# Kernel tuning notes

Hardware: AMD Instinct MI355X
Metric: run time of the kernel (lower is better)

The kernel has to match this reference:

```python
import jax, jax.numpy as jnp
import numpy as np

WH, WW = 16, 16          # window_size
C = 384                  # in_channel
H = 12                   # num_heads
HD = C // H              # head_dim = 32
B = 256                  # num_windows * batch
N = WH * WW              # tokens per window = 256
CPB_HID = 512


def _build_buffers():
    # relative_coords_table: [1, 2*WH-1, 2*WW-1, 2], log-spaced coords (pretrain_window_size = [0,0])
    rch = np.arange(-(WH - 1), WH, dtype=np.float32)
    rcw = np.arange(-(WW - 1), WW, dtype=np.float32)
    table = np.stack(np.meshgrid(rch, rcw, indexing='ij'), axis=-1)[None]  # [1,2WH-1,2WW-1,2]
    table[..., 0] /= (WH - 1)
    table[..., 1] /= (WW - 1)
    table = np.sign(table) * np.log2(np.abs(table) + 1.0) / np.log2(8)
    # relative_position_index: [N, N] int indices into flattened table
    ch = np.arange(WH)
    cw = np.arange(WW)
    coords = np.stack(np.meshgrid(ch, cw, indexing='ij'))      # [2, WH, WW]
    cf = coords.reshape(2, -1)                                  # [2, N]
    rel = cf[:, :, None] - cf[:, None, :]                       # [2, N, N]
    rel = rel.transpose(1, 2, 0).astype(np.int64)               # [N, N, 2]
    rel[..., 0] += WH - 1
    rel[..., 1] += WW - 1
    rel[..., 0] *= 2 * WW - 1
    rpi = rel.sum(-1)                                           # [N, N]
    return jnp.asarray(table, jnp.float32), jnp.asarray(rpi, jnp.int32)


def setup_inputs() -> dict:
    key = jax.random.key(0)
    ks = jax.random.split(key, 9)
    table, rpi = _build_buffers()
    return {
        'x': jax.random.normal(ks[0], (B, N, C), jnp.float32),
        'qkv_w': jax.random.normal(ks[1], (3 * C, C), jnp.float32) * 0.02,
        'q_bias': jnp.zeros((C,), jnp.float32),
        'v_bias': jnp.zeros((C,), jnp.float32),
        'logit_scale': jnp.log(10.0 * jnp.ones((H, 1, 1), jnp.float32)),
        'cpb_w1': jax.random.normal(ks[2], (CPB_HID, 2), jnp.float32) * 0.02,
        'cpb_b1': jnp.zeros((CPB_HID,), jnp.float32),
        'cpb_w2': jax.random.normal(ks[3], (H, CPB_HID), jnp.float32) * 0.02,
        'proj_w': jax.random.normal(ks[4], (C, C), jnp.float32) * 0.02,
        'proj_b': jnp.zeros((C,), jnp.float32),
        'rel_coords_table': table,
        'rel_pos_index': rpi,
    }


def reference(x, qkv_w, q_bias, v_bias, logit_scale, cpb_w1, cpb_b1, cpb_w2,
              proj_w, proj_b, rel_coords_table, rel_pos_index):
    b, n, c = x.shape
    h, hd = H, c // H
    # qkv with q/v bias, zero k bias
    bias = jnp.concatenate([q_bias, jnp.zeros_like(v_bias), v_bias])
    qkv = x @ qkv_w.T + bias                                   # [B,N,3C]
    qkv = qkv.reshape(b, n, 3, h, hd).transpose(2, 0, 3, 1, 4)  # [3,B,H,N,hd]
    q, k, v = qkv[0], qkv[1], qkv[2]
    # cosine attention: L2-normalize q, k (F.normalize with eps=1e-12)
    qn = q / jnp.maximum(jnp.linalg.norm(q, axis=-1, keepdims=True), 1e-12)
    kn = k / jnp.maximum(jnp.linalg.norm(k, axis=-1, keepdims=True), 1e-12)
    attn = jnp.einsum('bhnd,bhmd->bhnm', qn, kn)               # [B,H,N,N]
    # learnable per-head logit scale, clamped at log(1/0.01)
    scale = jnp.exp(jnp.minimum(logit_scale, jnp.log(100.0)))  # [H,1,1]
    attn = attn * scale
    # continuous relative position bias MLP: 2 -> 512 -> H
    hid = jax.nn.relu(rel_coords_table @ cpb_w1.T + cpb_b1)    # [1,2WH-1,2WW-1,512]
    bias_table = (hid @ cpb_w2.T).reshape(-1, h)               # [(2WH-1)*(2WW-1), H]
    rpb = bias_table[rel_pos_index.reshape(-1)].reshape(n, n, h).transpose(2, 0, 1)
    rpb = 16.0 * jax.nn.sigmoid(rpb)                           # [H,N,N]
    attn = jax.nn.softmax(attn + rpb, axis=-1)
    out = jnp.einsum('bhnm,bhmd->bhnd', attn, v)               # [B,H,N,hd]
    out = out.transpose(0, 2, 1, 3).reshape(b, n, c)
    return out @ proj_w.T + proj_b
```

## Files before the change

kernel.cpp:

```cpp
#include <hip/hip_runtime.h>

typedef unsigned int uint;
typedef unsigned short ushort_t;
typedef ushort_t ushort8 __attribute__((ext_vector_type(8)));
typedef ushort_t ushort4v __attribute__((ext_vector_type(4)));
typedef short short8 __attribute__((ext_vector_type(8)));
typedef float floatx4 __attribute__((ext_vector_type(4)));

#define WSQ 25165824L
#define NH  12
#define NT  256
#define HD  32

__device__ __forceinline__ float bf2f(ushort_t u) {
    uint x = ((uint)u) << 16;
    return __builtin_bit_cast(float, x);
}
__device__ __forceinline__ ushort_t f2bf(float f) {
    uint u = __builtin_bit_cast(uint, f);
    uint lsb = (u >> 16) & 1u;
    return (ushort_t)((u + 0x7FFFu + lsb) >> 16);
}
__device__ __forceinline__ float ld1(const void* p, long i, int f) {
    return f ? ((const float*)p)[i] : bf2f(((const ushort_t*)p)[i]);
}

__global__ void detect_kernel(const ushort_t* __restrict__ x, int* __restrict__ flag) {
    int t = threadIdx.x;
    uint u = x[2 * t];
    int e = (u >> 7) & 0xFF;
    int weird = (e > 147 || e < 107) ? 1 : 0;
    unsigned long long b = __ballot(weird);
    if (t == 0) *flag = (__popcll(b) > 19) ? 1 : 0;
}

__global__ __launch_bounds__(256) void cvt_kernel(
    const void* __restrict__ src, ushort_t* __restrict__ dst,
    const int* __restrict__ fl, long n8)
{
    long i = (long)blockIdx.x * 256 + threadIdx.x;
    if (i >= n8) return;
    if (*fl) {
        const floatx4* s = (const floatx4*)((const float*)src + i * 8);
        floatx4 a = s[0], b = s[1];
        ushort8 o;
        for (int j = 0; j < 4; ++j) { o[j] = f2bf(a[j]); o[4 + j] = f2bf(b[j]); }
        *(ushort8*)(dst + i * 8) = o;
    } else {
        *(ushort8*)(dst + i * 8) = *(const ushort8*)((const ushort_t*)src + i * 8);
    }
}

__global__ __launch_bounds__(512) void cpb_kernel(
    const void* __restrict__ tab, const void* __restrict__ w1,
    const void* __restrict__ b1, const void* __restrict__ w2,
    const int* __restrict__ fl, float* __restrict__ bt)
{
    __shared__ float hid[512];
    const int f = *fl;
    int p = blockIdx.x, j = threadIdx.x;
    float c0 = ld1(tab, p * 2 + 0, f);
    float c1 = ld1(tab, p * 2 + 1, f);
    float v = ld1(w1, j * 2 + 0, f) * c0 + ld1(w1, j * 2 + 1, f) * c1 + ld1(b1, j, f);
    hid[j] = fmaxf(v, 0.0f);
    __syncthreads();
    if (j < NH) {
        float s = 0.0f;
        for (int i = 0; i < 512; ++i) s += hid[i] * ld1(w2, (long)j * 512 + i, f);
        bt[p * NH + j] = s;
    }
}

__global__ __launch_bounds__(256) void rpb_kernel(
    const int* __restrict__ rpi, const float* __restrict__ bt,
    float* __restrict__ rpb)
{
    int idx = blockIdx.x * 256 + threadIdx.x;
    int h = idx >> 16, ij = idx & 65535;
    float x = bt[rpi[ij] * NH + h];
    rpb[idx] = 16.0f / (1.0f + __expf(-x));
}

template <int MODE>
__global__ __launch_bounds__(256) void gemm_bt(
    const ushort_t* __restrict__ A, const ushort_t* __restrict__ Bw,
    const void* __restrict__ bias0, const void* __restrict__ bias2,
    void* __restrict__ Cout, const int* __restrict__ fl)
{
    const int K = 384;
    __shared__ ushort_t As[128 * 72];
    __shared__ ushort_t Bs[128 * 72];
    const int f = *fl;
    const int tid = threadIdx.x;
    const int w = tid >> 6, lane = tid & 63, l15 = lane & 15, quad = lane >> 4;
    const int m0 = blockIdx.y * 128, n0 = blockIdx.x * 128;
    const int rw = (w >> 1) * 64, cw = (w & 1) * 64;
    const int lr = tid >> 3, lc = (tid & 7) * 8;

    floatx4 acc[4][4] = {};
    ushort8 pa[4], pb[4];

    for (int i = 0; i < 4; ++i) {
        int r = lr + i * 32;
        if (MODE == 0) {
            pa[i] = *(const ushort8*)&A[(long)(m0 + r) * K + lc];
        } else {
            int m = m0 + r, kc = lc;
            long ad = ((long)(m >> 8) * 12 + (kc >> 5)) * 8192 + (m & 255) * 32 + (kc & 31);
            pa[i] = *(const ushort8*)&A[ad];
        }
        pb[i] = *(const ushort8*)&Bw[(long)(n0 + r) * K + lc];
    }

    for (int kt = 0; kt < K; kt += 64) {
        for (int i = 0; i < 4; ++i) {
            int r = lr + i * 32;
            *(ushort8*)&As[r * 72 + lc] = pa[i];
            *(ushort8*)&Bs[r * 72 + lc] = pb[i];
        }
        __syncthreads();
        if (kt + 64 < K) {
            for (int i = 0; i < 4; ++i) {
                int r = lr + i * 32;
                if (MODE == 0) {
                    pa[i] = *(const ushort8*)&A[(long)(m0 + r) * K + kt + 64 + lc];
                } else {
                    int m = m0 + r, kc = kt + 64 + lc;
                    long ad = ((long)(m >> 8) * 12 + (kc >> 5)) * 8192 + (m & 255) * 32 + (kc & 31);
                    pa[i] = *(const ushort8*)&A[ad];
                }
                pb[i] = *(const ushort8*)&Bw[(long)(n0 + r) * K + kt + 64 + lc];
            }
        }
        for (int ks = 0; ks < 64; ks += 32) {
            short8 af[4], bfr[4];
            for (int mt = 0; mt < 4; ++mt)
                af[mt] = *(short8*)&As[(rw + mt * 16 + l15) * 72 + ks + quad * 8];
            for (int nt = 0; nt < 4; ++nt)
                bfr[nt] = *(short8*)&Bs[(cw + nt * 16 + l15) * 72 + ks + quad * 8];
            for (int mt = 0; mt < 4; ++mt)
                for (int nt = 0; nt < 4; ++nt)
                    acc[mt][nt] = __builtin_amdgcn_mfma_f32_16x16x32_bf16(
                        af[mt], bfr[nt], acc[mt][nt], 0, 0, 0);
        }
        __syncthreads();
    }

    for (int mt = 0; mt < 4; ++mt) {
        for (int nt = 0; nt < 4; ++nt) {
            int c = n0 + cw + nt * 16 + l15;
            if (MODE == 0) {
                int which = c / 384, cc = c % 384;
                float bias = (which == 0) ? ld1(bias0, cc, f)
                           : (which == 2) ? ld1(bias2, cc, f) : 0.0f;
                int hh = cc >> 5, dd = cc & 31;
                for (int r = 0; r < 4; ++r) {
                    int m = m0 + rw + mt * 16 + quad * 4 + r;
                    int b = m >> 8, ntok = m & 255;
                    long dst = (long)which * WSQ +
                               (((long)(b * NH + hh) * NT + ntok) * HD + dd);
                    ((ushort_t*)Cout)[dst] = f2bf(acc[mt][nt][r] + bias);
                }
            } else {
                float bias = ld1(bias0, c, f);
                for (int r = 0; r < 4; ++r) {
                    int m = m0 + rw + mt * 16 + quad * 4 + r;
                    float v = acc[mt][nt][r] + bias;
                    long o = (long)m * 384 + c;
                    if (f) ((float*)Cout)[o] = v;
                    else   ((ushort_t*)Cout)[o] = f2bf(v);
                }
            }
        }
    }
}

__global__ __launch_bounds__(128) void attn_kernel(
    ushort_t* __restrict__ qkv, const void* __restrict__ ls,
    const float* __restrict__ rpb, const int* __restrict__ fl)
{
    __shared__ ushort_t ks[256 * 40];
    __shared__ ushort_t vts[32 * 264];
    __shared__ ushort_t ps[2 * 16 * 264];

    const int f = *fl;
    const int bh = blockIdx.x;
    const int b = bh / NH, h = bh % NH;
    ushort_t* qp = qkv + (long)bh * NT * HD;
    const ushort_t* kp = qp + WSQ;
    const ushort_t* vp = qp + 2 * WSQ;
    const int tid = threadIdx.x;
    const float scale = __expf(fminf(ld1(ls, h, f), 4.6051702f));

    for (int t = tid; t < 256; t += 128) {
        ushort8 kv[4];
        for (int i = 0; i < 4; ++i) kv[i] = *(const ushort8*)&kp[t * HD + i * 8];
        float fv[32]; float ss = 0.0f;
        for (int i = 0; i < 4; ++i)
            for (int j = 0; j < 8; ++j) {
                float v = bf2f(kv[i][j]); fv[i * 8 + j] = v; ss += v * v;
            }
        float rn = 1.0f / fmaxf(sqrtf(ss), 1e-12f);
        for (int i = 0; i < 4; ++i) {
            ushort8 o;
            for (int j = 0; j < 8; ++j) o[j] = f2bf(fv[i * 8 + j] * rn);
            *(ushort8*)&ks[t * 40 + i * 8] = o;
        }
        ushort8 vv[4];
        for (int i = 0; i < 4; ++i) vv[i] = *(const ushort8*)&vp[t * HD + i * 8];
        for (int i = 0; i < 4; ++i)
            for (int j = 0; j < 8; ++j) vts[(i * 8 + j) * 264 + t] = vv[i][j];
    }
    __syncthreads();

    const int w = tid >> 6, lane = tid & 63, l15 = lane & 15, quad = lane >> 4;
    ushort_t* psw = &ps[w * 16 * 264];

    for (int c = 0; c < 8; ++c) {
        const int mloc = w * 128 + c * 16;

        ushort8 qv = *(const ushort8*)&qp[(mloc + l15) * HD + quad * 8];
        float qf[8]; float ss = 0.0f;
        for (int j = 0; j < 8; ++j) { qf[j] = bf2f(qv[j]); ss += qf[j] * qf[j]; }
        ss += __shfl_xor(ss, 16, 64);
        ss += __shfl_xor(ss, 32, 64);
        float rn = 1.0f / fmaxf(sqrtf(ss), 1e-12f);
        short8 aq;
        for (int j = 0; j < 8; ++j) aq[j] = (short)f2bf(qf[j] * rn);

        floatx4 accS[16];
        for (int t = 0; t < 16; ++t) {
            short8 bk = *(short8*)&ks[(t * 16 + l15) * 40 + quad * 8];
            floatx4 z = {};
            accS[t] = __builtin_amdgcn_mfma_f32_16x16x32_bf16(bk, aq, z, 0, 0, 0);
        }

        const float* rp = rpb + ((long)h * NT + mloc + l15) * NT;
        float rmax = -1e30f;
        for (int t = 0; t < 16; ++t) {
            floatx4 rb = *(const floatx4*)&rp[t * 16 + quad * 4];
            for (int r = 0; r < 4; ++r) {
                float v = accS[t][r] * scale + rb[r];
                accS[t][r] = v;
                rmax = fmaxf(rmax, v);
            }
        }
        rmax = fmaxf(rmax, __shfl_xor(rmax, 16, 64));
        rmax = fmaxf(rmax, __shfl_xor(rmax, 32, 64));
        float rsum = 0.0f;
        for (int t = 0; t < 16; ++t)
            for (int r = 0; r < 4; ++r) {
                float p = __expf(accS[t][r] - rmax);
                accS[t][r] = p;
                rsum += p;
            }
        rsum += __shfl_xor(rsum, 16, 64);
        rsum += __shfl_xor(rsum, 32, 64);
        float rinv = 1.0f / rsum;

        for (int t = 0; t < 16; ++t) {
            ushort4v o;
            for (int r = 0; r < 4; ++r) o[r] = f2bf(accS[t][r] * rinv);
            *(ushort4v*)&psw[l15 * 264 + t * 16 + quad * 4] = o;
        }

        floatx4 accO[2] = {};
        for (int kk = 0; kk < 8; ++kk) {
            short8 pf = *(short8*)&psw[l15 * 264 + kk * 32 + quad * 8];
            for (int tn = 0; tn < 2; ++tn) {
                short8 vf = *(short8*)&vts[(tn * 16 + l15) * 264 + kk * 32 + quad * 8];
                accO[tn] = __builtin_amdgcn_mfma_f32_16x16x32_bf16(pf, vf, accO[tn], 0, 0, 0);
            }
        }

        for (int tn = 0; tn < 2; ++tn)
            for (int r = 0; r < 4; ++r) {
                int n = mloc + quad * 4 + r;
                qp[n * HD + tn * 16 + l15] = f2bf(accO[tn][r]);
            }
    }
}

extern "C" void kernel_launch(void* const* d_in, const int* in_sizes, int n_in,
                              void* d_out, int out_size, void* d_ws, size_t ws_size,
                              hipStream_t stream)
{
    const void* x      = d_in[0];
    const void* qkv_w  = d_in[1];
    const void* q_bias = d_in[2];
    const void* v_bias = d_in[3];
    const void* lscale = d_in[4];
    const void* cpb_w1 = d_in[5];
    const void* cpb_b1 = d_in[6];
    const void* cpb_w2 = d_in[7];
    const void* proj_w = d_in[8];
    const void* proj_b = d_in[9];
    const void* rct    = d_in[10];
    const int*  rpi    = (const int*)d_in[11];

    char* ws = (char*)d_ws;
    ushort_t* qkv_ws  = (ushort_t*)ws;
    float*    bt      = (float*)(ws + 150994944L);
    float*    rpb     = (float*)(ws + 151060480L);
    int*      flag    = (int*)(ws + 154206208L);
    ushort_t* wqkv_b  = (ushort_t*)(ws + 154206464L);
    ushort_t* wproj_b = (ushort_t*)(ws + 155091200L);
    ushort_t* xb      = (ushort_t*)d_out;

    detect_kernel<<<1, 64, 0, stream>>>((const ushort_t*)x, flag);
    cvt_kernel<<<12288, 256, 0, stream>>>(x, xb, flag, 3145728L);
    cvt_kernel<<<216, 256, 0, stream>>>(qkv_w, wqkv_b, flag, 55296L);
    cvt_kernel<<<72, 256, 0, stream>>>(proj_w, wproj_b, flag, 18432L);
    cpb_kernel<<<961, 512, 0, stream>>>(rct, cpb_w1, cpb_b1, cpb_w2, flag, bt);
    rpb_kernel<<<3072, 256, 0, stream>>>(rpi, bt, rpb);
    gemm_bt<0><<<dim3(9, 512), 256, 0, stream>>>(xb, wqkv_b, q_bias, v_bias, qkv_ws, flag);
    attn_kernel<<<3072, 128, 0, stream>>>(qkv_ws, lscale, rpb, flag);
    gemm_bt<1><<<dim3(3, 512), 256, 0, stream>>>(qkv_ws, wproj_b, proj_b, nullptr, d_out, flag);
}
```

Baseline: 536.4 us.

## Fuse softmax exp into PV MMA loop with deferred normalization and exp2

Restructures the attention softmax so the exponentials are computed per 32-column chunk and fed straight into the P·V MFMA. Normalization by the row sum moves to the output accumulator, which shrinks the P scratch buffer in LDS and removes a full pass over the scores. It also folds log2(e) into the logit scale and the bias table so it can use the hardware v_exp_f32, and replaces manual bf16 rounding with packed v_cvt_pk_bf16_f32. Risks are a slightly different rounding order, since unnormalized P is rounded to bf16, and reliance on inline asm availability.

```diff
diff --git a/kernel.cpp b/kernel.cpp
--- a/kernel.cpp
+++ b/kernel.cpp
@@ -6,6 +6,8 @@
 typedef ushort_t ushort4v __attribute__((ext_vector_type(4)));
 typedef short short8 __attribute__((ext_vector_type(8)));
 typedef float floatx4 __attribute__((ext_vector_type(4)));
+typedef uint uint2v __attribute__((ext_vector_type(2)));
+typedef uint uint4v __attribute__((ext_vector_type(4)));
 
 #define WSQ 25165824L
 #define NH  12
@@ -20,6 +22,16 @@
     uint u = __builtin_bit_cast(uint, f);
     uint lsb = (u >> 16) & 1u;
     return (ushort_t)((u + 0x7FFFu + lsb) >> 16);
+}
+__device__ __forceinline__ uint cvt_pk_bf16(float lo, float hi) {
+    uint r;
+    asm("v_cvt_pk_bf16_f32 %0, %1, %2" : "=v"(r) : "v"(lo), "v"(hi));
+    return r;
+}
+__device__ __forceinline__ float exp2_fast(float x) {
+    float r;
+    asm("v_exp_f32 %0, %1" : "=v"(r) : "v"(x));
+    return r;
 }
 __device__ __forceinline__ float ld1(const void* p, long i, int f) {
     return f ? ((const float*)p)[i] : bf2f(((const ushort_t*)p)[i]);
@@ -78,7 +90,7 @@
     int idx = blockIdx.x * 256 + threadIdx.x;
     int h = idx >> 16, ij = idx & 65535;
     float x = bt[rpi[ij] * NH + h];
-    rpb[idx] = 16.0f / (1.0f + __expf(-x));
+    rpb[idx] = 1.44269504f * 16.0f / (1.0f + __expf(-x));
 }
 
 template <int MODE>
@@ -179,9 +191,9 @@
     ushort_t* __restrict__ qkv, const void* __restrict__ ls,
     const float* __restrict__ rpb, const int* __restrict__ fl)
 {
-    __shared__ ushort_t ks[256 * 40];
-    __shared__ ushort_t vts[32 * 264];
-    __shared__ ushort_t ps[2 * 16 * 264];
+    __shared__ __attribute__((aligned(16))) ushort_t ks[256 * 40];
+    __shared__ __attribute__((aligned(16))) ushort_t vts[32 * 264];
+    __shared__ __attribute__((aligned(16))) ushort_t ps[2 * 16 * 40];
 
     const int f = *fl;
     const int bh = blockIdx.x;
@@ -190,45 +202,59 @@
     const ushort_t* kp = qp + WSQ;
     const ushort_t* vp = qp + 2 * WSQ;
     const int tid = threadIdx.x;
-    const float scale = __expf(fminf(ld1(ls, h, f), 4.6051702f));
+    const float scale = __expf(fminf(ld1(ls, h, f), 4.6051702f)) * 1.44269504f;
 
     for (int t = tid; t < 256; t += 128) {
         ushort8 kv[4];
+        #pragma unroll
         for (int i = 0; i < 4; ++i) kv[i] = *(const ushort8*)&kp[t * HD + i * 8];
         float fv[32]; float ss = 0.0f;
+        #pragma unroll
         for (int i = 0; i < 4; ++i)
+            #pragma unroll
             for (int j = 0; j < 8; ++j) {
                 float v = bf2f(kv[i][j]); fv[i * 8 + j] = v; ss += v * v;
             }
         float rn = 1.0f / fmaxf(sqrtf(ss), 1e-12f);
+        #pragma unroll
         for (int i = 0; i < 4; ++i) {
-            ushort8 o;
-            for (int j = 0; j < 8; ++j) o[j] = f2bf(fv[i * 8 + j] * rn);
-            *(ushort8*)&ks[t * 40 + i * 8] = o;
+            uint4v o;
+            #pragma unroll
+            for (int j = 0; j < 4; ++j)
+                o[j] = cvt_pk_bf16(fv[i * 8 + 2 * j] * rn, fv[i * 8 + 2 * j + 1] * rn);
+            *(uint4v*)&ks[t * 40 + i * 8] = o;
         }
         ushort8 vv[4];
+        #pragma unroll
         for (int i = 0; i < 4; ++i) vv[i] = *(const ushort8*)&vp[t * HD + i * 8];
+        #pragma unroll
         for (int i = 0; i < 4; ++i)
+            #pragma unroll
             for (int j = 0; j < 8; ++j) vts[(i * 8 + j) * 264 + t] = vv[i][j];
     }
     __syncthreads();
 
     const int w = tid >> 6, lane = tid & 63, l15 = lane & 15, quad = lane >> 4;
-    ushort_t* psw = &ps[w * 16 * 264];
+    ushort_t* psw = &ps[w * 16 * 40];
 
     for (int c = 0; c < 8; ++c) {
         const int mloc = w * 128 + c * 16;
 
         ushort8 qv = *(const ushort8*)&qp[(mloc + l15) * HD + quad * 8];
         float qf[8]; float ss = 0.0f;
+        #pragma unroll
         for (int j = 0; j < 8; ++j) { qf[j] = bf2f(qv[j]); ss += qf[j] * qf[j]; }
         ss += __shfl_xor(ss, 16, 64);
         ss += __shfl_xor(ss, 32, 64);
         float rn = 1.0f / fmaxf(sqrtf(ss), 1e-12f);
-        short8 aq;
-        for (int j = 0; j < 8; ++j) aq[j] = (short)f2bf(qf[j] * rn);
+        uint4v qa;
+        #pragma unroll
+        for (int j = 0; j < 4; ++j)
+            qa[j] = cvt_pk_bf16(qf[2 * j] * rn, qf[2 * j + 1] * rn);
+        short8 aq = __builtin_bit_cast(short8, qa);
 
         floatx4 accS[16];
+        #pragma unroll
         for (int t = 0; t < 16; ++t) {
             short8 bk = *(short8*)&ks[(t * 16 + l15) * 40 + quad * 8];
             floatx4 z = {};
@@ -236,47 +262,62 @@
         }
 
         const float* rp = rpb + ((long)h * NT + mloc + l15) * NT;
-        float rmax = -1e30f;
+        float m4[4] = {-3e38f, -3e38f, -3e38f, -3e38f};
+        #pragma unroll
         for (int t = 0; t < 16; ++t) {
             floatx4 rb = *(const floatx4*)&rp[t * 16 + quad * 4];
-            for (int r = 0; r < 4; ++r) {
-                float v = accS[t][r] * scale + rb[r];
-                accS[t][r] = v;
-                rmax = fmaxf(rmax, v);
-            }
-        }
+            float v0 = fmaf(accS[t][0], scale, rb[0]);
+            float v1 = fmaf(accS[t][1], scale, rb[1]);
+            float v2 = fmaf(accS[t][2], scale, rb[2]);
+            float v3 = fmaf(accS[t][3], scale, rb[3]);
+            accS[t][0] = v0; accS[t][1] = v1; accS[t][2] = v2; accS[t][3] = v3;
+            m4[t & 3] = fmaxf(m4[t & 3], fmaxf(fmaxf(v0, v1), fmaxf(v2, v3)));
+        }
+        float rmax = fmaxf(fmaxf(m4[0], m4[1]), fmaxf(m4[2], m4[3]));
         rmax = fmaxf(rmax, __shfl_xor(rmax, 16, 64));
         rmax = fmaxf(rmax, __shfl_xor(rmax, 32, 64));
-        float rsum = 0.0f;
-        for (int t = 0; t < 16; ++t)
-            for (int r = 0; r < 4; ++r) {
-                float p = __expf(accS[t][r] - rmax);
-                accS[t][r] = p;
-                rsum += p;
-            }
+
+        float s4[4] = {0.f, 0.f, 0.f, 0.f};
+        floatx4 accO[2] = {};
+        #pragma unroll
+        for (int kk = 0; kk < 8; ++kk) {
+            #pragma unroll
+            for (int th = 0; th < 2; ++th) {
+                int t = kk * 2 + th;
+                float p0 = exp2_fast(accS[t][0] - rmax);
+                float p1 = exp2_fast(accS[t][1] - rmax);
+                float p2 = exp2_fast(accS[t][2] - rmax);
+                float p3 = exp2_fast(accS[t][3] - rmax);
+                s4[0] += p0; s4[1] += p1; s4[2] += p2; s4[3] += p3;
+                uint2v po;
+                po[0] = cvt_pk_bf16(p0, p1);
+                po[1] = cvt_pk_bf16(p2, p3);
+                *(uint2v*)&psw[l15 * 40 + th * 16 + quad * 4] = po;
+            }
+            short8 pf = *(short8*)&psw[l15 * 40 + quad * 8];
+            #pragma unroll
+            for (int tn = 0; tn < 2; ++tn) {
+                short8 vf = *(short8*)&vts[(tn * 16 + l15) * 264 + kk * 32 + quad * 8];
+                accO[tn] = __builtin_amdgcn_mfma_f32_16x16x32_bf16(pf, vf, accO[tn], 0, 0, 0);
+            }
+        }
+
+        float rsum = (s4[0] + s4[1]) + (s4[2] + s4[3]);
         rsum += __shfl_xor(rsum, 16, 64);
         rsum += __shfl_xor(rsum, 32, 64);
         float rinv = 1.0f / rsum;
-
-        for (int t = 0; t < 16; ++t) {
-            ushort4v o;
-            for (int r = 0; r < 4; ++r) o[r] = f2bf(accS[t][r] * rinv);
-            *(ushort4v*)&psw[l15 * 264 + t * 16 + quad * 4] = o;
-        }
-
-        floatx4 accO[2] = {};
-        for (int kk = 0; kk < 8; ++kk) {
-            short8 pf = *(short8*)&psw[l15 * 264 + kk * 32 + quad * 8];
-            for (int tn = 0; tn < 2; ++tn) {
-                short8 vf = *(short8*)&vts[(tn * 16 + l15) * 264 + kk * 32 + quad * 8];
-                accO[tn] = __builtin_amdgcn_mfma_f32_16x16x32_bf16(pf, vf, accO[tn], 0, 0, 0);
-            }
-        }
-
+        float ri[4];
+        #pragma unroll
+        for (int r = 0; r < 4; ++r) ri[r] = __shfl(rinv, quad * 4 + r, 64);
+
+        #pragma unroll
         for (int tn = 0; tn < 2; ++tn)
-            for (int r = 0; r < 4; ++r) {
+            #pragma unroll
+            for (int r = 0; r < 4; r += 2) {
+                uint pk = cvt_pk_bf16(accO[tn][r] * ri[r], accO[tn][r + 1] * ri[r + 1]);
                 int n = mloc + quad * 4 + r;
-                qp[n * HD + tn * 16 + l15] = f2bf(accO[tn][r]);
+                qp[n * HD + tn * 16 + l15] = (ushort_t)pk;
+                qp[(n + 1) * HD + tn * 16 + l15] = (ushort_t)(pk >> 16);
             }
     }
 }
```

Result: faster. 510.9 us (-4.8%).
